# Performance work log

Measured on AMD Instinct MI355X. Metric: run time of the kernel, lower is better.

Reference implementation:

```python
import jax, jax.numpy as jnp
import numpy as np


def _relative_position_index(wd, wh, ww):
    coords = np.stack(np.meshgrid(np.arange(wd), np.arange(wh), np.arange(ww), indexing='ij'))
    flat = coords.reshape(3, -1)                      # (3, N)
    rel = flat[:, :, None] - flat[:, None, :]         # (3, N, N)
    rel = rel.transpose(1, 2, 0).astype(np.int64)     # (N, N, 3)
    rel[..., 0] += wd - 1
    rel[..., 1] += wh - 1
    rel[..., 2] += ww - 1
    rel[..., 0] *= (2 * wh - 1) * (2 * ww - 1)
    rel[..., 1] *= (2 * ww - 1)
    return rel.sum(-1)                                 # (N, N)


def setup_inputs() -> dict:
    key = jax.random.key(0)
    k0, k1, k2, k3 = jax.random.split(key, 4)
    B, D, H, W = 4, 16, 56, 56
    wd, wh, ww = 8, 7, 7
    C, nH = 128, 4
    N = wd * wh * ww                                   # 392
    nW = (D // wd) * (H // wh) * (W // ww)             # 128
    B_ = B * nW                                        # 512
    table_sz = (2 * wd - 1) * (2 * wh - 1) * (2 * ww - 1)  # 2535
    x = jax.random.normal(k0, (B_, N, C), jnp.float32)
    mask = jnp.zeros((nW, N, N), jnp.float32)          # 0/-inf additive mask; zeros = no shift
    qkv_w = jax.random.normal(k1, (3 * C, C), jnp.float32) * 0.02
    proj_w = jax.random.normal(k2, (C, C), jnp.float32) * 0.02
    proj_b = jnp.zeros((C,), jnp.float32)
    bias_table = jax.random.normal(k3, (table_sz, nH), jnp.float32) * 0.02
    rel_index = jnp.asarray(_relative_position_index(wd, wh, ww), jnp.int32)
    return {"x": x, "mask": mask, "qkv_w": qkv_w, "proj_w": proj_w,
            "proj_b": proj_b, "bias_table": bias_table, "rel_index": rel_index}


def reference(x, mask, qkv_w, proj_w, proj_b, bias_table, rel_index):
    B_, N, C = x.shape
    nH = bias_table.shape[1]
    hd = C // nH
    scale = hd ** -0.5
    # qkv projection (no bias, qkv_bias=False)
    qkv = (x @ qkv_w.T).reshape(B_, N, 3, nH, hd).transpose(2, 0, 3, 1, 4)  # (3,B_,H,N,hd)
    q, k, v = qkv[0] * scale, qkv[1], qkv[2]
    attn = jnp.einsum('bhnd,bhmd->bhnm', q, k)                              # (B_,H,N,N)
    bias = bias_table[rel_index.reshape(-1)].reshape(N, N, nH).transpose(2, 0, 1)
    attn = attn + bias[None]
    nW = mask.shape[0]
    attn = attn.reshape(B_ // nW, nW, nH, N, N) + mask[None, :, None]
    attn = jax.nn.softmax(attn.reshape(B_, nH, N, N), axis=-1)
    out = jnp.einsum('bhnm,bhmd->bhnd', attn, v)                            # (B_,H,N,hd)
    out = out.transpose(0, 2, 1, 3).reshape(B_, N, C)
    return out @ proj_w.T + proj_b
```

## Files before the change

### kernel.cpp

```cpp
#include <hip/hip_runtime.h>

typedef unsigned short u16;
typedef unsigned int   u32;

#define NTOK   392
#define NN2    153664
#define QSCALE 0.17677669529663687f
#define LOG2E  1.44269504088896340736f

typedef __attribute__((ext_vector_type(8))) __bf16 bf16x8;
typedef __attribute__((ext_vector_type(4))) float  f32x4;
#define MFMA16(a,b,c) __builtin_amdgcn_mfma_f32_16x16x32_bf16((a),(b),(c),0,0,0)

__device__ __forceinline__ float bf2f(u16 u){
    union { u32 i; float f; } v; v.i = ((u32)u) << 16; return v.f;
}
__device__ __forceinline__ u16 f2bf(float x){
    union { float f; u32 i; } v; v.f = x;
    u32 r = (v.i + 0x7FFFu + ((v.i >> 16) & 1u)) >> 16;
    return (u16)r;
}
__device__ __forceinline__ float ldf(const void* p, int isb, long i){
    if (isb) return bf2f(((const u16*)p)[i]);
    else     return ((const float*)p)[i];
}
__device__ __forceinline__ void stf(void* p, int isb, long i, float v){
    if (isb) ((u16*)p)[i] = f2bf(v);
    else     ((float*)p)[i] = v;
}

__device__ __forceinline__ void ld8s(const void* p, int isb, long i0,
                                     bf16x8* h, bf16x8* l){
    union { u16 u[8]; bf16x8 v; } H, L;
    if (isb){
        const uint2* q = (const uint2*)((const u16*)p + i0);
        uint2 a = q[0], b = q[1];
        H.u[0]=(u16)a.x; H.u[1]=(u16)(a.x>>16); H.u[2]=(u16)a.y; H.u[3]=(u16)(a.y>>16);
        H.u[4]=(u16)b.x; H.u[5]=(u16)(b.x>>16); H.u[6]=(u16)b.y; H.u[7]=(u16)(b.y>>16);
        #pragma unroll
        for (int j = 0; j < 8; ++j) L.u[j] = 0;
    } else {
        const float4* q = (const float4*)((const float*)p + i0);
        float4 a = q[0], b = q[1];
        float f[8] = {a.x,a.y,a.z,a.w,b.x,b.y,b.z,b.w};
        #pragma unroll
        for (int j = 0; j < 8; ++j){
            u16 hh = f2bf(f[j]);
            H.u[j] = hh;
            L.u[j] = f2bf(f[j] - bf2f(hh));
        }
    }
    *h = H.v; *l = L.v;
}

__device__ __forceinline__ int plaus(u16 w){
    int e = (w >> 7) & 0xFF;
    return (w == 0) || (e >= 96 && e <= 145);
}
__global__ __launch_bounds__(256) void prep_kernel(
        const u16* __restrict__ x, int* __restrict__ flags){
    __shared__ int cnt[2];
    int tid = threadIdx.x;
    if (tid < 2) cnt[tid] = 0;
    __syncthreads();
    int p = plaus(x[tid]) + plaus(x[tid + 256]);
    if (p) atomicAdd(&cnt[0], p);
    int ez = ((tid & 1) == 0 && x[tid] == 0) + (((tid + 256) & 1) == 0 && x[tid + 256] == 0);
    if (ez) atomicAdd(&cnt[1], ez);
    __syncthreads();
    if (tid == 0){
        flags[0] = (cnt[1] < 64 && cnt[0] >= 436) ? 1 : 0;
        flags[4] = 0;
    }
}

__global__ __launch_bounds__(256) void mask_scan_kernel(
        const u32* __restrict__ m, int nhalf, const int* __restrict__ flagsRO,
        int* __restrict__ flags){
    long nw = flagsRO[0] ? nhalf : 2L * nhalf;
    long i0 = (long)blockIdx.x * 256 + threadIdx.x;
    u32 acc = 0;
    for (long i = i0; i < nw; i += (long)gridDim.x * 256) acc |= m[i];
    if (acc) atomicOr(&flags[4], 1);
}

__global__ __launch_bounds__(256) void bias_expand_kernel(
        const int* __restrict__ rel_index, const void* btabP,
        const int* __restrict__ flags, float* __restrict__ biasfull){
    int idx = blockIdx.x * 256 + threadIdx.x;
    int isb = flags[0];
    if (idx < NN2){
        int t = rel_index[idx];
        #pragma unroll
        for (int h = 0; h < 4; ++h)
            biasfull[(long)h * NN2 + idx] = ldf(btabP, isb, (long)t * 4 + h);
    }
}

__global__ __launch_bounds__(512) void attn_mfma_kernel(
        const void* xP, const void* qwP, const void* maskP,
        const float* __restrict__ biasfull, const int* __restrict__ flags,
        void* outP){
    __shared__ __align__(16) u16 Qh[400 * 40];
    __shared__ __align__(16) u16 Kh[416 * 40];
    __shared__ __align__(16) u16 VT[32 * 424];
    __shared__ __align__(16) u16 uni[2 * 64 * 136];

    u16* xs_hi = uni;
    u16* xs_lo = uni + 64 * 136;

    const int tid  = threadIdx.x;
    const int lane = tid & 63;
    const int wv   = tid >> 6;
    const int c    = lane & 15;
    const int g    = lane >> 4;
    const int h    = blockIdx.x;
    const int b_   = blockIdx.y;
    const int wdx  = b_ & 127;
    const int isb  = flags[0], fm = flags[4];
    const long xbase = (long)b_ * NTOK * 128;

    for (int i = tid; i < 32 * 32; i += 512){
        int d = i >> 5;
        VT[d * 424 + 392 + (i & 31)] = 0;
    }

    const int mt  = wv >> 1;
    const int ntb = (wv & 1) * 3;
    bf16x8 WH[3][4], WL[3][4];
    #pragma unroll
    for (int j = 0; j < 3; ++j){
        int n = (ntb + j) * 16 + c;
        int wrow = (n < 32) ? (h * 32 + n)
                 : (n < 64) ? (128 + h * 32 + (n - 32))
                 :            (256 + h * 32 + (n - 64));
        #pragma unroll
        for (int ks = 0; ks < 4; ++ks)
            ld8s(qwP, isb, (long)wrow * 128 + ks * 32 + 8 * g, &WH[j][ks], &WL[j][ks]);
    }

    for (int ch = 0; ch < 7; ++ch){
        const int tok0 = ch * 64;
        __syncthreads();
        #pragma unroll
        for (int jj = 0; jj < 4; ++jj){
            int idx = jj * 2048 + tid * 4;
            int r = idx >> 7, cc = idx & 127;
            int row = tok0 + r;
            u32 h01, h23, l01, l23;
            if (row < NTOK){
                long gi = xbase + (long)row * 128 + cc;
                if (isb){
                    uint2 a = *(const uint2*)((const u16*)xP + gi);
                    h01 = a.x; h23 = a.y; l01 = 0; l23 = 0;
                } else {
                    float4 f = *(const float4*)((const float*)xP + gi);
                    u16 h0=f2bf(f.x), h1=f2bf(f.y), h2=f2bf(f.z), h3=f2bf(f.w);
                    h01 = h0 | ((u32)h1 << 16); h23 = h2 | ((u32)h3 << 16);
                    l01 = (u32)f2bf(f.x - bf2f(h0)) | ((u32)f2bf(f.y - bf2f(h1)) << 16);
                    l23 = (u32)f2bf(f.z - bf2f(h2)) | ((u32)f2bf(f.w - bf2f(h3)) << 16);
                }
            } else { h01 = h23 = l01 = l23 = 0; }
            *(uint2*)&xs_hi[r * 136 + cc] = make_uint2(h01, h23);
            *(uint2*)&xs_lo[r * 136 + cc] = make_uint2(l01, l23);
        }
        __syncthreads();
        #pragma unroll
        for (int j = 0; j < 3; ++j){
            f32x4 acc = {0.f, 0.f, 0.f, 0.f};
            #pragma unroll
            for (int ks = 0; ks < 4; ++ks){
                bf16x8 ah = *(const bf16x8*)&xs_hi[(mt * 16 + c) * 136 + ks * 32 + 8 * g];
                bf16x8 al = *(const bf16x8*)&xs_lo[(mt * 16 + c) * 136 + ks * 32 + 8 * g];
                acc = MFMA16(ah, WH[j][ks], acc);
                acc = MFMA16(al, WH[j][ks], acc);
                acc = MFMA16(ah, WL[j][ks], acc);
            }
            int n = (ntb + j) * 16 + c;
            #pragma unroll
            for (int i = 0; i < 4; ++i){
                int tok = tok0 + mt * 16 + 4 * g + i;
                if (tok < NTOK){
                    if (n < 32)      Qh[tok * 40 + n]         = f2bf(acc[i] * QSCALE);
                    else if (n < 64) Kh[tok * 40 + (n - 32)]  = f2bf(acc[i]);
                    else             VT[(n - 64) * 424 + tok] = f2bf(acc[i]);
                }
            }
        }
    }
    __syncthreads();

    u16* pb = uni + wv * 640;
    for (int qt = wv; qt < 25; qt += 8){
        const int q0 = qt * 16;
        bf16x8 qa = *(const bf16x8*)&Qh[(q0 + c) * 40 + 8 * g];
        f32x4 o0 = {0.f,0.f,0.f,0.f}, o1 = {0.f,0.f,0.f,0.f};
        float rs0 = 0.f, rs1 = 0.f, rs2 = 0.f, rs3 = 0.f;
        int qr[4];
        #pragma unroll
        for (int i = 0; i < 4; ++i){
            int q = q0 + 4 * g + i;
            qr[i] = (q < NTOK) ? q : (NTOK - 1);
        }
        const float* bptr = biasfull + (long)h * NN2;
        float bn0 = bptr[(long)qr[0] * NTOK + c];
        float bn1 = bptr[(long)qr[1] * NTOK + c];
        float bn2 = bptr[(long)qr[2] * NTOK + c];
        float bn3 = bptr[(long)qr[3] * NTOK + c];
        for (int kt = 0; kt < 26; ++kt){
            bf16x8 kb = *(const bf16x8*)&Kh[(kt * 16 + c) * 40 + 8 * g];
            f32x4 z = {0.f,0.f,0.f,0.f};
            f32x4 s = MFMA16(qa, kb, z);
            float b0 = bn0, b1 = bn1, b2 = bn2, b3 = bn3;
            if (kt < 25){
                int keyn = (kt + 1) * 16 + c; if (keyn >= NTOK) keyn = NTOK - 1;
                bn0 = bptr[(long)qr[0] * NTOK + keyn];
                bn1 = bptr[(long)qr[1] * NTOK + keyn];
                bn2 = bptr[(long)qr[2] * NTOK + keyn];
                bn3 = bptr[(long)qr[3] * NTOK + keyn];
            }
            int key = kt * 16 + c;
            if (fm){
                long mb = (long)wdx * NN2;
                int kc = (key < NTOK) ? key : (NTOK - 1);
                b0 += ldf(maskP, isb, mb + (long)qr[0] * NTOK + kc);
                b1 += ldf(maskP, isb, mb + (long)qr[1] * NTOK + kc);
                b2 += ldf(maskP, isb, mb + (long)qr[2] * NTOK + kc);
                b3 += ldf(maskP, isb, mb + (long)qr[3] * NTOK + kc);
            }
            bool kvld = key < NTOK;
            float p0 = kvld ? exp2f((s[0] + b0) * LOG2E) : 0.f;
            float p1 = kvld ? exp2f((s[1] + b1) * LOG2E) : 0.f;
            float p2 = kvld ? exp2f((s[2] + b2) * LOG2E) : 0.f;
            float p3 = kvld ? exp2f((s[3] + b3) * LOG2E) : 0.f;
            rs0 += p0; rs1 += p1; rs2 += p2; rs3 += p3;
            int co = (kt & 1) * 16 + c;
            pb[(4 * g + 0) * 40 + co] = f2bf(p0);
            pb[(4 * g + 1) * 40 + co] = f2bf(p1);
            pb[(4 * g + 2) * 40 + co] = f2bf(p2);
            pb[(4 * g + 3) * 40 + co] = f2bf(p3);
            if (kt & 1){
                bf16x8 pa = *(const bf16x8*)&pb[c * 40 + 8 * g];
                int kk = (kt >> 1) * 32 + 8 * g;
                bf16x8 v0 = *(const bf16x8*)&VT[c * 424 + kk];
                bf16x8 v1 = *(const bf16x8*)&VT[(c + 16) * 424 + kk];
                o0 = MFMA16(pa, v0, o0);
                o1 = MFMA16(pa, v1, o1);
            }
        }
        #pragma unroll
        for (int m = 1; m < 16; m <<= 1){
            rs0 += __shfl_xor(rs0, m, 64);
            rs1 += __shfl_xor(rs1, m, 64);
            rs2 += __shfl_xor(rs2, m, 64);
            rs3 += __shfl_xor(rs3, m, 64);
        }
        float inv[4] = {1.f / rs0, 1.f / rs1, 1.f / rs2, 1.f / rs3};
        #pragma unroll
        for (int i = 0; i < 4; ++i){
            int tok = q0 + 4 * g + i;
            if (tok < NTOK){
                stf(outP, isb, xbase + (long)tok * 128 + h * 32 + c,      o0[i] * inv[i]);
                stf(outP, isb, xbase + (long)tok * 128 + h * 32 + 16 + c, o1[i] * inv[i]);
            }
        }
    }
}

__global__ __launch_bounds__(512) void proj_mfma_kernel(
        const void* wP, const void* bP, const int* __restrict__ flags,
        void* outP){
    __shared__ __align__(16) u16 xs_hi[64 * 136];
    __shared__ __align__(16) u16 xs_lo[64 * 136];
    const int tid  = threadIdx.x;
    const int lane = tid & 63;
    const int wv   = tid >> 6;
    const int c    = lane & 15;
    const int g    = lane >> 4;
    const int isb  = flags[0];
    const long m0  = (long)blockIdx.x * 64;

    #pragma unroll
    for (int jj = 0; jj < 4; ++jj){
        int idx = jj * 2048 + tid * 4;
        int r = idx >> 7, cc = idx & 127;
        long gi = (m0 + r) * 128 + cc;
        u32 h01, h23, l01, l23;
        if (isb){
            uint2 a = *(const uint2*)((const u16*)outP + gi);
            h01 = a.x; h23 = a.y; l01 = 0; l23 = 0;
        } else {
            float4 f = *(const float4*)((const float*)outP + gi);
            u16 h0=f2bf(f.x), h1=f2bf(f.y), h2=f2bf(f.z), h3=f2bf(f.w);
            h01 = h0 | ((u32)h1 << 16); h23 = h2 | ((u32)h3 << 16);
            l01 = (u32)f2bf(f.x - bf2f(h0)) | ((u32)f2bf(f.y - bf2f(h1)) << 16);
            l23 = (u32)f2bf(f.z - bf2f(h2)) | ((u32)f2bf(f.w - bf2f(h3)) << 16);
        }
        *(uint2*)&xs_hi[r * 136 + cc] = make_uint2(h01, h23);
        *(uint2*)&xs_lo[r * 136 + cc] = make_uint2(l01, l23);
    }
    __syncthreads();
    const int mt  = wv >> 1;
    const int ntb = (wv & 1) * 4;
    bf16x8 ah[4], al[4];
    #pragma unroll
    for (int ks = 0; ks < 4; ++ks){
        ah[ks] = *(const bf16x8*)&xs_hi[(mt * 16 + c) * 136 + ks * 32 + 8 * g];
        al[ks] = *(const bf16x8*)&xs_lo[(mt * 16 + c) * 136 + ks * 32 + 8 * g];
    }
    #pragma unroll
    for (int j = 0; j < 4; ++j){
        int nt = ntb + j;
        bf16x8 wh[4], wl[4];
        #pragma unroll
        for (int ks = 0; ks < 4; ++ks)
            ld8s(wP, isb, (long)(nt * 16 + c) * 128 + ks * 32 + 8 * g, &wh[ks], &wl[ks]);
        f32x4 acc = {0.f,0.f,0.f,0.f};
        #pragma unroll
        for (int ks = 0; ks < 4; ++ks){
            acc = MFMA16(ah[ks], wh[ks], acc);
            acc = MFMA16(al[ks], wh[ks], acc);
            acc = MFMA16(ah[ks], wl[ks], acc);
        }
        float bias = ldf(bP, isb, nt * 16 + c);
        #pragma unroll
        for (int i = 0; i < 4; ++i){
            long row = m0 + mt * 16 + 4 * g + i;
            stf(outP, isb, row * 128 + nt * 16 + c, acc[i] + bias);
        }
    }
}

extern "C" void kernel_launch(void* const* d_in, const int* in_sizes, int n_in,
                              void* d_out, int out_size, void* d_ws, size_t ws_size,
                              hipStream_t stream){
    const void* x      = d_in[0];
    const void* mask   = d_in[1];
    const void* qkv_w  = d_in[2];
    const void* proj_w = d_in[3];
    const void* proj_b = d_in[4];
    const void* btab   = d_in[5];
    const int*  relidx = (const int*)d_in[6];

    int*   flags    = (int*)d_ws;
    float* biasfull = (float*)((char*)d_ws + 256);

    prep_kernel<<<dim3(1), dim3(256), 0, stream>>>((const u16*)x, flags);
    int nhalf = in_sizes[1] / 2;
    mask_scan_kernel<<<dim3(2048), dim3(256), 0, stream>>>(
        (const u32*)mask, nhalf, flags, flags);
    bias_expand_kernel<<<dim3((NN2 + 255) / 256), dim3(256), 0, stream>>>(
        relidx, btab, flags, biasfull);
    attn_mfma_kernel<<<dim3(4, 512), dim3(512), 0, stream>>>(
        x, qkv_w, mask, biasfull, flags, d_out);
    proj_mfma_kernel<<<dim3(3136), dim3(512), 0, stream>>>(
        proj_w, proj_b, flags, d_out);
}
```

Before: 823.1 us.

## Restructure attention inner loop with transposed padded bias and two query tiles per wave

Measured after the change: 719.8 us. 12.5% less time.

```diff
diff --git a/kernel.cpp b/kernel.cpp
--- a/kernel.cpp
+++ b/kernel.cpp
@@ -5,8 +5,10 @@
 
 #define NTOK   392
 #define NN2    153664
-#define QSCALE 0.17677669529663687f
 #define LOG2E  1.44269504088896340736f
+#define QSCL   (0.17677669529663687f * 1.44269504088896340736f)
+#define BTQ    416
+#define BTH    (416L*416L)
 
 typedef __attribute__((ext_vector_type(8))) __bf16 bf16x8;
 typedef __attribute__((ext_vector_type(4))) float  f32x4;
@@ -19,6 +21,9 @@
     union { float f; u32 i; } v; v.f = x;
     u32 r = (v.i + 0x7FFFu + ((v.i >> 16) & 1u)) >> 16;
     return (u16)r;
+}
+__device__ __forceinline__ u16 bfbits(float x){
+    union { __bf16 b; u16 u; } v; v.b = (__bf16)x; return v.u;
 }
 __device__ __forceinline__ float ldf(const void* p, int isb, long i){
     if (isb) return bf2f(((const u16*)p)[i]);
@@ -86,22 +91,33 @@
 
 __global__ __launch_bounds__(256) void bias_expand_kernel(
         const int* __restrict__ rel_index, const void* btabP,
-        const int* __restrict__ flags, float* __restrict__ biasfull){
-    int idx = blockIdx.x * 256 + threadIdx.x;
+        const int* __restrict__ flags, float* __restrict__ biasT){
+    long idx = (long)blockIdx.x * 256 + threadIdx.x;
+    if (idx >= BTH) return;
+    int key = (int)(idx / BTQ);
+    int q   = (int)(idx - (long)key * BTQ);
     int isb = flags[0];
-    if (idx < NN2){
-        int t = rel_index[idx];
-        #pragma unroll
-        for (int h = 0; h < 4; ++h)
-            biasfull[(long)h * NN2 + idx] = ldf(btabP, isb, (long)t * 4 + h);
-    }
+    float v0, v1, v2, v3;
+    if (key >= NTOK){ v0 = v1 = v2 = v3 = -1e30f; }
+    else if (q >= NTOK){ v0 = v1 = v2 = v3 = 0.f; }
+    else {
+        int t = rel_index[(long)q * NTOK + key];
+        v0 = ldf(btabP, isb, (long)t * 4 + 0) * LOG2E;
+        v1 = ldf(btabP, isb, (long)t * 4 + 1) * LOG2E;
+        v2 = ldf(btabP, isb, (long)t * 4 + 2) * LOG2E;
+        v3 = ldf(btabP, isb, (long)t * 4 + 3) * LOG2E;
+    }
+    biasT[0 * BTH + idx] = v0;
+    biasT[1 * BTH + idx] = v1;
+    biasT[2 * BTH + idx] = v2;
+    biasT[3 * BTH + idx] = v3;
 }
 
 __global__ __launch_bounds__(512) void attn_mfma_kernel(
         const void* xP, const void* qwP, const void* maskP,
-        const float* __restrict__ biasfull, const int* __restrict__ flags,
+        const float* __restrict__ biasT, const int* __restrict__ flags,
         void* outP){
-    __shared__ __align__(16) u16 Qh[400 * 40];
+    __shared__ __align__(16) u16 Qh[416 * 40];
     __shared__ __align__(16) u16 Kh[416 * 40];
     __shared__ __align__(16) u16 VT[32 * 424];
     __shared__ __align__(16) u16 uni[2 * 64 * 136];
@@ -114,16 +130,14 @@
     const int wv   = tid >> 6;
     const int c    = lane & 15;
     const int g    = lane >> 4;
-    const int h    = blockIdx.x;
-    const int b_   = blockIdx.y;
+    const int h    = blockIdx.y;
+    const int b_   = blockIdx.x;
     const int wdx  = b_ & 127;
     const int isb  = flags[0], fm = flags[4];
     const long xbase = (long)b_ * NTOK * 128;
 
-    for (int i = tid; i < 32 * 32; i += 512){
-        int d = i >> 5;
-        VT[d * 424 + 392 + (i & 31)] = 0;
-    }
+    for (int i = tid; i < 24 * 40; i += 512){ Qh[392 * 40 + i] = 0; Kh[392 * 40 + i] = 0; }
+    for (int i = tid; i < 32 * 32; i += 512) VT[(i >> 5) * 424 + 392 + (i & 31)] = 0;
 
     const int mt  = wv >> 1;
     const int ntb = (wv & 1) * 3;
@@ -181,7 +195,7 @@
             for (int i = 0; i < 4; ++i){
                 int tok = tok0 + mt * 16 + 4 * g + i;
                 if (tok < NTOK){
-                    if (n < 32)      Qh[tok * 40 + n]         = f2bf(acc[i] * QSCALE);
+                    if (n < 32)      Qh[tok * 40 + n]         = f2bf(acc[i] * QSCL);
                     else if (n < 64) Kh[tok * 40 + (n - 32)]  = f2bf(acc[i]);
                     else             VT[(n - 64) * 424 + tok] = f2bf(acc[i]);
                 }
@@ -190,78 +204,124 @@
     }
     __syncthreads();
 
-    u16* pb = uni + wv * 640;
-    for (int qt = wv; qt < 25; qt += 8){
-        const int q0 = qt * 16;
-        bf16x8 qa = *(const bf16x8*)&Qh[(q0 + c) * 40 + 8 * g];
-        f32x4 o0 = {0.f,0.f,0.f,0.f}, o1 = {0.f,0.f,0.f,0.f};
-        float rs0 = 0.f, rs1 = 0.f, rs2 = 0.f, rs3 = 0.f;
-        int qr[4];
-        #pragma unroll
-        for (int i = 0; i < 4; ++i){
-            int q = q0 + 4 * g + i;
-            qr[i] = (q < NTOK) ? q : (NTOK - 1);
-        }
-        const float* bptr = biasfull + (long)h * NN2;
-        float bn0 = bptr[(long)qr[0] * NTOK + c];
-        float bn1 = bptr[(long)qr[1] * NTOK + c];
-        float bn2 = bptr[(long)qr[2] * NTOK + c];
-        float bn3 = bptr[(long)qr[3] * NTOK + c];
-        for (int kt = 0; kt < 26; ++kt){
-            bf16x8 kb = *(const bf16x8*)&Kh[(kt * 16 + c) * 40 + 8 * g];
-            f32x4 z = {0.f,0.f,0.f,0.f};
-            f32x4 s = MFMA16(qa, kb, z);
-            float b0 = bn0, b1 = bn1, b2 = bn2, b3 = bn3;
-            if (kt < 25){
-                int keyn = (kt + 1) * 16 + c; if (keyn >= NTOK) keyn = NTOK - 1;
-                bn0 = bptr[(long)qr[0] * NTOK + keyn];
-                bn1 = bptr[(long)qr[1] * NTOK + keyn];
-                bn2 = bptr[(long)qr[2] * NTOK + keyn];
-                bn3 = bptr[(long)qr[3] * NTOK + keyn];
-            }
-            int key = kt * 16 + c;
-            if (fm){
-                long mb = (long)wdx * NN2;
-                int kc = (key < NTOK) ? key : (NTOK - 1);
-                b0 += ldf(maskP, isb, mb + (long)qr[0] * NTOK + kc);
-                b1 += ldf(maskP, isb, mb + (long)qr[1] * NTOK + kc);
-                b2 += ldf(maskP, isb, mb + (long)qr[2] * NTOK + kc);
-                b3 += ldf(maskP, isb, mb + (long)qr[3] * NTOK + kc);
-            }
-            bool kvld = key < NTOK;
-            float p0 = kvld ? exp2f((s[0] + b0) * LOG2E) : 0.f;
-            float p1 = kvld ? exp2f((s[1] + b1) * LOG2E) : 0.f;
-            float p2 = kvld ? exp2f((s[2] + b2) * LOG2E) : 0.f;
-            float p3 = kvld ? exp2f((s[3] + b3) * LOG2E) : 0.f;
-            rs0 += p0; rs1 += p1; rs2 += p2; rs3 += p3;
-            int co = (kt & 1) * 16 + c;
-            pb[(4 * g + 0) * 40 + co] = f2bf(p0);
-            pb[(4 * g + 1) * 40 + co] = f2bf(p1);
-            pb[(4 * g + 2) * 40 + co] = f2bf(p2);
-            pb[(4 * g + 3) * 40 + co] = f2bf(p3);
-            if (kt & 1){
-                bf16x8 pa = *(const bf16x8*)&pb[c * 40 + 8 * g];
-                int kk = (kt >> 1) * 32 + 8 * g;
+    u16* pbA = uni + wv * 1280;
+    u16* pbB = pbA + 640;
+    const float* bT = biasT + (long)h * BTH;
+    const long mb = (long)wdx * NN2;
+
+    for (int task = wv; task < 13; task += 8){
+        const int qa0 = task * 32;
+        const int qb0 = qa0 + 16;
+        bf16x8 qA = *(const bf16x8*)&Qh[(qa0 + c) * 40 + 8 * g];
+        bf16x8 qB = *(const bf16x8*)&Qh[(qb0 + c) * 40 + 8 * g];
+        f32x4 oA0={0.f,0.f,0.f,0.f}, oA1={0.f,0.f,0.f,0.f};
+        f32x4 oB0={0.f,0.f,0.f,0.f}, oB1={0.f,0.f,0.f,0.f};
+        float rsA0=0.f,rsA1=0.f,rsA2=0.f,rsA3=0.f;
+        float rsB0=0.f,rsB1=0.f,rsB2=0.f,rsB3=0.f;
+        const float* bp = bT + (long)c * BTQ + qa0 + 4 * g;
+        f32x4 rA0 = *(const f32x4*)(bp);
+        f32x4 rB0 = *(const f32x4*)(bp + 16);
+        f32x4 rA1 = *(const f32x4*)(bp + 16 * BTQ);
+        f32x4 rB1 = *(const f32x4*)(bp + 16 * BTQ + 16);
+        const float* fp = bp + 32 * BTQ;
+
+        for (int k2 = 0; k2 < 13; ++k2){
+            {
+                const int kt = 2 * k2;
+                bf16x8 kb = *(const bf16x8*)&Kh[(kt * 16 + c) * 40 + 8 * g];
+                f32x4 cA = rA0, cB = rB0;
+                if (k2 < 12){
+                    rA0 = *(const f32x4*)(fp);
+                    rB0 = *(const f32x4*)(fp + 16);
+                }
+                if (fm){
+                    int key = kt * 16 + c; int kc = key < NTOK ? key : NTOK - 1;
+                    #pragma unroll
+                    for (int i = 0; i < 4; ++i){
+                        int qa_ = qa0 + 4 * g + i; if (qa_ >= NTOK) qa_ = NTOK - 1;
+                        int qb_ = qb0 + 4 * g + i; if (qb_ >= NTOK) qb_ = NTOK - 1;
+                        cA[i] += ldf(maskP, isb, mb + (long)qa_ * NTOK + kc) * LOG2E;
+                        cB[i] += ldf(maskP, isb, mb + (long)qb_ * NTOK + kc) * LOG2E;
+                    }
+                }
+                f32x4 sA = MFMA16(qA, kb, cA);
+                f32x4 sB = MFMA16(qB, kb, cB);
+                float pA[4], pB[4];
+                #pragma unroll
+                for (int i = 0; i < 4; ++i){ pA[i] = exp2f(sA[i]); pB[i] = exp2f(sB[i]); }
+                rsA0 += pA[0]; rsA1 += pA[1]; rsA2 += pA[2]; rsA3 += pA[3];
+                rsB0 += pB[0]; rsB1 += pB[1]; rsB2 += pB[2]; rsB3 += pB[3];
+                #pragma unroll
+                for (int i = 0; i < 4; ++i){
+                    pbA[(4 * g + i) * 40 + c] = bfbits(pA[i]);
+                    pbB[(4 * g + i) * 40 + c] = bfbits(pB[i]);
+                }
+            }
+            {
+                const int kt = 2 * k2 + 1;
+                bf16x8 kb = *(const bf16x8*)&Kh[(kt * 16 + c) * 40 + 8 * g];
+                f32x4 cA = rA1, cB = rB1;
+                if (k2 < 12){
+                    rA1 = *(const f32x4*)(fp + 16 * BTQ);
+                    rB1 = *(const f32x4*)(fp + 16 * BTQ + 16);
+                    fp += 32 * BTQ;
+                }
+                if (fm){
+                    int key = kt * 16 + c; int kc = key < NTOK ? key : NTOK - 1;
+                    #pragma unroll
+                    for (int i = 0; i < 4; ++i){
+                        int qa_ = qa0 + 4 * g + i; if (qa_ >= NTOK) qa_ = NTOK - 1;
+                        int qb_ = qb0 + 4 * g + i; if (qb_ >= NTOK) qb_ = NTOK - 1;
+                        cA[i] += ldf(maskP, isb, mb + (long)qa_ * NTOK + kc) * LOG2E;
+                        cB[i] += ldf(maskP, isb, mb + (long)qb_ * NTOK + kc) * LOG2E;
+                    }
+                }
+                f32x4 sA = MFMA16(qA, kb, cA);
+                f32x4 sB = MFMA16(qB, kb, cB);
+                float pA[4], pB[4];
+                #pragma unroll
+                for (int i = 0; i < 4; ++i){ pA[i] = exp2f(sA[i]); pB[i] = exp2f(sB[i]); }
+                rsA0 += pA[0]; rsA1 += pA[1]; rsA2 += pA[2]; rsA3 += pA[3];
+                rsB0 += pB[0]; rsB1 += pB[1]; rsB2 += pB[2]; rsB3 += pB[3];
+                #pragma unroll
+                for (int i = 0; i < 4; ++i){
+                    pbA[(4 * g + i) * 40 + 16 + c] = bfbits(pA[i]);
+                    pbB[(4 * g + i) * 40 + 16 + c] = bfbits(pB[i]);
+                }
+                bf16x8 paA = *(const bf16x8*)&pbA[c * 40 + 8 * g];
+                bf16x8 paB = *(const bf16x8*)&pbB[c * 40 + 8 * g];
+                int kk = k2 * 32 + 8 * g;
                 bf16x8 v0 = *(const bf16x8*)&VT[c * 424 + kk];
                 bf16x8 v1 = *(const bf16x8*)&VT[(c + 16) * 424 + kk];
-                o0 = MFMA16(pa, v0, o0);
-                o1 = MFMA16(pa, v1, o1);
-            }
-        }
+                oA0 = MFMA16(paA, v0, oA0);
+                oA1 = MFMA16(paA, v1, oA1);
+                oB0 = MFMA16(paB, v0, oB0);
+                oB1 = MFMA16(paB, v1, oB1);
+            }
+        }
+        float rsA[4] = {rsA0, rsA1, rsA2, rsA3};
+        float rsB[4] = {rsB0, rsB1, rsB2, rsB3};
         #pragma unroll
         for (int m = 1; m < 16; m <<= 1){
-            rs0 += __shfl_xor(rs0, m, 64);
-            rs1 += __shfl_xor(rs1, m, 64);
-            rs2 += __shfl_xor(rs2, m, 64);
-            rs3 += __shfl_xor(rs3, m, 64);
-        }
-        float inv[4] = {1.f / rs0, 1.f / rs1, 1.f / rs2, 1.f / rs3};
+            #pragma unroll
+            for (int i = 0; i < 4; ++i){
+                rsA[i] += __shfl_xor(rsA[i], m, 64);
+                rsB[i] += __shfl_xor(rsB[i], m, 64);
+            }
+        }
         #pragma unroll
         for (int i = 0; i < 4; ++i){
-            int tok = q0 + 4 * g + i;
-            if (tok < NTOK){
-                stf(outP, isb, xbase + (long)tok * 128 + h * 32 + c,      o0[i] * inv[i]);
-                stf(outP, isb, xbase + (long)tok * 128 + h * 32 + 16 + c, o1[i] * inv[i]);
+            int ta = qa0 + 4 * g + i;
+            if (ta < NTOK){
+                float ia = 1.f / rsA[i];
+                stf(outP, isb, xbase + (long)ta * 128 + h * 32 + c,      oA0[i] * ia);
+                stf(outP, isb, xbase + (long)ta * 128 + h * 32 + 16 + c, oA1[i] * ia);
+            }
+            int tb = qb0 + 4 * g + i;
+            if (tb < NTOK){
+                float ib = 1.f / rsB[i];
+                stf(outP, isb, xbase + (long)tb * 128 + h * 32 + c,      oB0[i] * ib);
+                stf(outP, isb, xbase + (long)tb * 128 + h * 32 + 16 + c, oB1[i] * ib);
             }
         }
     }
@@ -342,17 +402,17 @@
     const void* btab   = d_in[5];
     const int*  relidx = (const int*)d_in[6];
 
-    int*   flags    = (int*)d_ws;
-    float* biasfull = (float*)((char*)d_ws + 256);
+    int*   flags = (int*)d_ws;
+    float* biasT = (float*)((char*)d_ws + 256);
 
     prep_kernel<<<dim3(1), dim3(256), 0, stream>>>((const u16*)x, flags);
     int nhalf = in_sizes[1] / 2;
     mask_scan_kernel<<<dim3(2048), dim3(256), 0, stream>>>(
         (const u32*)mask, nhalf, flags, flags);
-    bias_expand_kernel<<<dim3((NN2 + 255) / 256), dim3(256), 0, stream>>>(
-        relidx, btab, flags, biasfull);
-    attn_mfma_kernel<<<dim3(4, 512), dim3(512), 0, stream>>>(
-        x, qkv_w, mask, biasfull, flags, d_out);
+    bias_expand_kernel<<<dim3((int)((BTH + 255) / 256)), dim3(256), 0, stream>>>(
+        relidx, btab, flags, biasT);
+    attn_mfma_kernel<<<dim3(512, 4), dim3(512), 0, stream>>>(
+        x, qkv_w, mask, biasT, flags, d_out);
     proj_mfma_kernel<<<dim3(3136), dim3(512), 0, stream>>>(
         proj_w, proj_b, flags, d_out);
 }
```
